# Optimization experiments

Hardware: AMD Instinct MI355X
Metric: run time of the kernel (lower is better)

The kernel has to match this reference:

```python
import jax, jax.numpy as jnp
import numpy as np

B, L, D, H, T = 1024, 50, 4, 512, 30


def _lstm_cell(x, h, c, W_ih, W_hh, b_ih, b_hh):
    # PyTorch LSTM gate order: i, f, g, o
    g = x @ W_ih.T + b_ih + h @ W_hh.T + b_hh
    i, f, gg, o = jnp.split(g, 4, axis=-1)
    c = jax.nn.sigmoid(f) * c + jax.nn.sigmoid(i) * jnp.tanh(gg)
    h = jax.nn.sigmoid(o) * jnp.tanh(c)
    return h, c


def setup_inputs() -> dict:
    key = jax.random.key(0)
    ks = jax.random.split(key, 16)
    s = 0.05
    return {
        "input_tensor": jax.random.normal(ks[0], (B, L, D), jnp.float32),
        "target_len": T,
        "enc_W_ih": jax.random.normal(ks[1], (4 * H, D), jnp.float32) * s,
        "enc_W_hh": jax.random.normal(ks[2], (4 * H, H), jnp.float32) * s,
        "enc_b_ih": jax.random.normal(ks[3], (4 * H,), jnp.float32) * s,
        "enc_b_hh": jax.random.normal(ks[4], (4 * H,), jnp.float32) * s,
        "attn_W": jax.random.normal(ks[5], (L, H + D), jnp.float32) * s,
        "attn_b": jax.random.normal(ks[6], (L,), jnp.float32) * s,
        "comb_W": jax.random.normal(ks[7], (H, H + D), jnp.float32) * s,
        "comb_b": jax.random.normal(ks[8], (H,), jnp.float32) * s,
        "dec_W_ih": jax.random.normal(ks[9], (4 * H, H), jnp.float32) * s,
        "dec_W_hh": jax.random.normal(ks[10], (4 * H, H), jnp.float32) * s,
        "dec_b_ih": jax.random.normal(ks[11], (4 * H,), jnp.float32) * s,
        "dec_b_hh": jax.random.normal(ks[12], (4 * H,), jnp.float32) * s,
        "out_W": jax.random.normal(ks[13], (D, H), jnp.float32) * s,
        "out_b": jax.random.normal(ks[14], (D,), jnp.float32) * s,
    }


def reference(input_tensor, target_len, enc_W_ih, enc_W_hh, enc_b_ih, enc_b_hh,
              attn_W, attn_b, comb_W, comb_b,
              dec_W_ih, dec_W_hh, dec_b_ih, dec_b_hh, out_W, out_b):
    b = input_tensor.shape[0]

    # ---- encoder LSTM over input_len steps ----
    def enc_step(carry, x_t):
        h, c = carry
        h, c = _lstm_cell(x_t, h, c, enc_W_ih, enc_W_hh, enc_b_ih, enc_b_hh)
        return (h, c), h

    h0 = jnp.zeros((b, H), input_tensor.dtype)
    (h_enc, c_enc), enc_hs = jax.lax.scan(enc_step, (h0, h0),
                                          jnp.swapaxes(input_tensor, 0, 1))
    encoder_outputs = jnp.swapaxes(enc_hs, 0, 1)  # [B, L, H]

    # ---- recursive attention decoder over target_len steps ----
    def dec_step(carry, _):
        h, c, x = carry
        # faithful to torch: h.reshape(h.shape[1], -1).transpose(1, 0)
        h_r = jnp.transpose(h.reshape(H, -1))  # [B, H] (memory reinterpret)
        attn_logits = jnp.concatenate([x, h_r], axis=1) @ attn_W.T + attn_b
        attn_weights = jax.nn.softmax(attn_logits, axis=1)        # [B, L]
        attn_applied = jnp.einsum('bl,blh->bh', attn_weights, encoder_outputs)
        comb = jnp.concatenate([x, attn_applied], axis=1) @ comb_W.T + comb_b
        comb = jax.nn.relu(comb)                                  # [B, H]
        h, c = _lstm_cell(comb, h, c, dec_W_ih, dec_W_hh, dec_b_ih, dec_b_hh)
        pred = h @ out_W.T + out_b                                # [B, D]
        return (h, c, pred), pred

    dec_in0 = input_tensor[:, -1, :]
    _, preds = jax.lax.scan(dec_step, (h_enc, c_enc, dec_in0), None,
                            length=target_len)
    return jnp.swapaxes(preds, 0, 1)  # [B, target_len, D]
```

## Files before the change

### kernel.cpp

```cpp
#include <hip/hip_runtime.h>
#include <hip/hip_bf16.h>

#define Bsz   1024
#define Lseq  50
#define Din   4
#define Hd    512
#define Tlen  30
#define NWG   256

typedef __hip_bfloat16 bf16;
typedef short s16x8 __attribute__((ext_vector_type(8)));
typedef short s16x4 __attribute__((ext_vector_type(4)));
typedef float f32x4 __attribute__((ext_vector_type(4)));
typedef int   i32x2 __attribute__((ext_vector_type(2)));

__device__ __forceinline__ float bf2f(bf16 x){ return __bfloat162float(x); }
__device__ __forceinline__ bf16  f2bf(float x){ return __float2bfloat16(x); }
__device__ __forceinline__ float bfbits2f(short u){
    union { unsigned int ui; float f; } v;
    v.ui = ((unsigned int)(unsigned short)u) << 16;
    return v.f;
}
__device__ __forceinline__ short f2bfbits(float x){
    bf16 h = f2bf(x); short s; __builtin_memcpy(&s, &h, 2); return s;
}
__device__ __forceinline__ float sigm(float x){ return 1.0f/(1.0f + __expf(-x)); }
__device__ __forceinline__ float ftanh(float x){
    const float e = __expf(2.0f*x);
    return 1.0f - 2.0f/(e + 1.0f);
}
__device__ __forceinline__ i32x2 pack4(float a, float b, float c, float d){
    i32x2 v;
    v[0] = (int)(unsigned short)f2bfbits(a) | ((int)(unsigned short)f2bfbits(b) << 16);
    v[1] = (int)(unsigned short)f2bfbits(c) | ((int)(unsigned short)f2bfbits(d) << 16);
    return v;
}
__device__ __forceinline__ s16x4 sc_load_b64(const void* p){
    i32x2 v;
    asm volatile("global_load_dwordx2 %0, %1, off sc0 sc1\n\ts_waitcnt vmcnt(0)"
                 : "=v"(v) : "v"(p) : "memory");
    s16x4 r; __builtin_memcpy(&r, &v, 8); return r;
}

#define OFF_ABUF0   (0u)
#define OFF_ABUF1   (2u<<20)
#define OFF_ATTNAP  (8u<<20)
#define OFF_XDEC    (9u<<20)
#define OFF_FLAG    ((9u<<20) + (16u<<10))
#define OFF_COMBWR  ((9u<<20) + (32u<<10))
#define OFF_ATTNWR  ((9u<<20) + (600u<<10))
#define OFF_FLAGS   ((9u<<20) + (704u<<10))
#define OFF_WCACHE  (10u<<20)
#define OFF_ENCOUT  (18u<<20)

#define WC_INPUT 0
#define WC_EWIH  204800
#define WC_EWHH  212992
#define WC_EBIH  1261568
#define WC_EBHH  1263616
#define WC_AW    1265664
#define WC_AB    1291464
#define WC_CW    1291520
#define WC_CB    1555712
#define WC_DWIH  1556224
#define WC_DWHH  2604800
#define WC_DBIH  3653376
#define WC_DBHH  3655424
#define WC_OW    3657472
#define WC_OB    3659520
#define WC_TOTAL 3659524

__device__ __constant__ int WOFF[15] = {
    WC_INPUT, WC_EWIH, WC_EWHH, WC_EBIH, WC_EBHH, WC_AW, WC_AB, WC_CW,
    WC_CB, WC_DWIH, WC_DWHH, WC_DBIH, WC_DBHH, WC_OW, WC_OB };
__device__ __constant__ int WNUM[15] = {
    204800, 8192, 1048576, 2048, 2048, 25800, 50, 264192,
    512, 1048576, 1048576, 2048, 2048, 2048, 4 };

struct Ptrs15 { const void* p[15]; };

__global__ void probe_kernel(const unsigned int* __restrict__ w, int* flag){
    __shared__ int cnt;
    if (threadIdx.x == 0) cnt = 0;
    __syncthreads();
    int c = 0;
    for (int i = threadIdx.x; i < 4096; i += 256){
        unsigned e = (w[i] >> 7) & 0xFFu;
        c += (e >= 0x80u) ? 1 : 0;
    }
    atomicAdd(&cnt, c);
    __syncthreads();
    if (threadIdx.x == 0) *flag = (cnt > 400) ? 1 : 0;
}

__global__ __launch_bounds__(256) void convert_kernel(
    Ptrs15 srcs, const int* __restrict__ flag, bf16* __restrict__ dst)
{
    const int f = *flag;
    for (int idx = blockIdx.x*256 + threadIdx.x; idx < WC_TOTAL;
         idx += gridDim.x*256){
        int a = 0;
#pragma unroll
        for (int j = 1; j < 15; ++j) if (idx >= WOFF[j]) a = j;
        const int local = idx - WOFF[a];
        if (local >= WNUM[a]) continue;
        bf16 v;
        if (f) v = f2bf(((const float*)srcs.p[a])[local]);
        else   v = ((const bf16*)srcs.p[a])[local];
        dst[idx] = v;
    }
}

__global__ __launch_bounds__(256) void setup_kernel(
    bf16* __restrict__ Abuf0, bf16* __restrict__ Abuf1,
    bf16* __restrict__ combWr, bf16* __restrict__ attnWr,
    const bf16* __restrict__ cWc, const bf16* __restrict__ aWc)
{
    const unsigned idx = blockIdx.x*256u + threadIdx.x;
    if (idx < (unsigned)Bsz*Hd){
        const unsigned row = idx >> 9, col = idx & (Hd-1);
        const bf16 z = f2bf(0.0f);
        Abuf0[(size_t)row*1024 + Hd + col] = z;
        Abuf1[(size_t)row*1024 + Hd + col] = z;
    }
    if (idx < (unsigned)Hd*Hd)
        combWr[idx] = cWc[(size_t)(idx >> 9)*(Hd+Din) + Din + (idx & (Hd-1))];
    if (idx < (unsigned)Lseq*Hd)
        attnWr[idx] = aWc[(size_t)(idx >> 9)*(Hd+Din) + Din + (idx & (Hd-1))];
}

struct MegaP {
    const bf16 *input, *eWih, *eWhh, *ebih, *ebhh;
    const bf16 *aW, *ab, *cW, *cb, *dWih, *dWhh, *dbih, *dbhh, *oW, *ob;
    const bf16 *combWr, *attnWr;
    bf16 *A0, *A1, *encout, *attnap, *xdec;
    int *wflag, *gflag, *xccmap;
    const int *flag;
    void *dout;
};

#define WSTRIDE 536

__global__ __launch_bounds__(512, 2) void mega_kernel(MegaP P)
{
    __shared__ short w1_lds[64*WSTRIDE];
    __shared__ short w2_lds[64*WSTRIDE];
    __shared__ short hr_s[4][Hd];
    __shared__ float ctx_s[2][4][8][64];
    __shared__ float aw_s[4][64];
    __shared__ int   xmap_s[NWG];
    __shared__ int   info_s[2];

    const int wg = blockIdx.x, tid = threadIdx.x;
    const int wave = tid >> 6, lane = tid & 63;
    const int quad = lane >> 4, l15 = lane & 15;
    const int lbase = lane & ~3;
    const int f32out = *P.flag;

    const int grp = wg & 7, rank = wg >> 3;

    int ep = 0;

    auto flag_round = [&](bool fence){
        ++ep;
        __syncthreads();
        if (tid == 0){
            if (fence) __threadfence();
            __hip_atomic_store(P.wflag + wg*16, ep, __ATOMIC_RELAXED, __HIP_MEMORY_SCOPE_SYSTEM);
        }
        if (rank == 0){
            if (tid < 32){
                int* f = P.wflag + (tid*8 + grp)*16;
                while (__hip_atomic_load(f, __ATOMIC_RELAXED, __HIP_MEMORY_SCOPE_SYSTEM) < ep)
                    __builtin_amdgcn_s_sleep(1);
            }
            __syncthreads();
            if (tid == 0)
                __hip_atomic_store(P.gflag + grp*16, ep, __ATOMIC_RELAXED, __HIP_MEMORY_SCOPE_SYSTEM);
        }
        if (tid < 8){
            int* f = P.gflag + tid*16;
            while (__hip_atomic_load(f, __ATOMIC_RELAXED, __HIP_MEMORY_SCOPE_SYSTEM) < ep)
                __builtin_amdgcn_s_sleep(1);
        }
        __syncthreads();
    };

    auto GSYNCF = [&](){
        flag_round(true);
        asm volatile("buffer_inv sc0 sc1" ::: "memory");
        __syncthreads();
    };

    if (tid == 0){
        int xcc = 0;
        asm volatile("s_getreg_b32 %0, hwreg(HW_REG_XCC_ID)" : "=s"(xcc));
        P.xccmap[wg] = xcc & 7;
    }
    GSYNCF();
    if (tid < NWG) xmap_s[tid] = P.xccmap[tid];
    __syncthreads();
    if (tid == 0){
        int ok = 1;
        for (int g = 0; g < 8; ++g){
            const int x0 = xmap_s[g];
            for (int i = 1; i < 32; ++i) ok &= (xmap_s[i*8 + g] == x0);
        }
        info_s[0] = ok;
    }
    __syncthreads();
    const int bal = info_s[0];

    auto GSYNCL = [&](){
        if (!bal){ GSYNCF(); return; }
        flag_round(true);
        asm volatile("buffer_inv" ::: "memory");
        __syncthreads();
    };
    auto XSYNC = [&](){
        if (!bal){ GSYNCF(); return; }
        ++ep;
        __syncthreads();
        if (tid == 0)
            __hip_atomic_store(P.wflag + wg*16, ep, __ATOMIC_RELAXED, __HIP_MEMORY_SCOPE_SYSTEM);
        if (tid < 32){
            int* f = P.wflag + (tid*8 + grp)*16;
            while (__hip_atomic_load(f, __ATOMIC_RELAXED, __HIP_MEMORY_SCOPE_SYSTEM) < ep)
                __builtin_amdgcn_s_sleep(1);
        }
        __syncthreads();
        asm volatile("buffer_inv" ::: "memory");
    };

    bf16* bufs[2] = { P.A0, P.A1 };

    const int bm0 = grp*128, hc0 = rank*16;
    const int wm = wave >> 1, wn = wave & 1;
    const int arow0 = bm0 + wm*32 + l15;

    int ng[2];
#pragma unroll
    for (int nf = 0; nf < 2; ++nf){
        const int n = wn*32 + nf*16 + l15;
        ng[nf] = (n & 3)*Hd + hc0 + (n >> 2);
    }

    float bias_e[2], wxv_e[2][4];
#pragma unroll
    for (int nf = 0; nf < 2; ++nf){
        bias_e[nf] = bf2f(P.ebih[ng[nf]]) + bf2f(P.ebhh[ng[nf]]);
        const s16x4 t4 = *reinterpret_cast<const s16x4*>(P.eWih + (size_t)ng[nf]*Din);
#pragma unroll
        for (int d = 0; d < 4; ++d) wxv_e[nf][d] = bfbits2f(t4[d]);
    }

    for (int i = tid; i < 64*64; i += 512){
        const int col = i >> 6, k8 = (i & 63)*8;
        const int g = (col & 3)*Hd + hc0 + (col >> 2);
        const s16x8 v = *reinterpret_cast<const s16x8*>(P.eWhh + (size_t)g*Hd + k8);
        *reinterpret_cast<s16x8*>(&w2_lds[col*WSTRIDE + k8]) = v;
    }
    __syncthreads();

    float creg[2][2][4];
#pragma unroll
    for (int a = 0; a < 2; ++a)
#pragma unroll
        for (int b = 0; b < 2; ++b)
#pragma unroll
            for (int r = 0; r < 4; ++r) creg[a][b][r] = 0.0f;

    for (int t = 0; t < Lseq; ++t){
        const bf16* Ain = bufs[t&1] + Hd;
        bf16* hout = bufs[(t+1)&1] + Hd;

        f32x4 acc[2][2];
#pragma unroll
        for (int mf=0; mf<2; ++mf)
#pragma unroll
            for (int nf=0; nf<2; ++nf) acc[mf][nf] = (f32x4)0.0f;

        s16x8 afr[2], bfr[2];
#pragma unroll
        for (int sl = 0; sl < 16; ++sl){
#pragma unroll
            for (int mf = 0; mf < 2; ++mf)
                afr[mf] = *reinterpret_cast<const s16x8*>(
                    Ain + (size_t)(arow0 + mf*16)*1024 + sl*32 + quad*8);
#pragma unroll
            for (int nf = 0; nf < 2; ++nf){
                const int nl = wn*32 + nf*16 + l15;
                bfr[nf] = *reinterpret_cast<const s16x8*>(
                    &w2_lds[nl*WSTRIDE + sl*32 + quad*8]);
            }
#pragma unroll
            for (int mf = 0; mf < 2; ++mf)
#pragma unroll
                for (int nf = 0; nf < 2; ++nf)
                    acc[mf][nf] = __builtin_amdgcn_mfma_f32_16x16x32_bf16(
                        afr[mf], bfr[nf], acc[mf][nf], 0, 0, 0);
        }

#pragma unroll
        for (int mf = 0; mf < 2; ++mf){
#pragma unroll
            for (int r = 0; r < 4; ++r){
                const int m = bm0 + wm*32 + mf*16 + quad*4 + r;
                const s16x4 xt = *reinterpret_cast<const s16x4*>(
                    P.input + ((size_t)m*Lseq + t)*Din);
                float xv[4];
#pragma unroll
                for (int d = 0; d < 4; ++d) xv[d] = bfbits2f(xt[d]);
#pragma unroll
                for (int nf = 0; nf < 2; ++nf){
                    const int n_loc = wn*32 + nf*16 + l15;
                    float gv = acc[mf][nf][r] + bias_e[nf]
                             + xv[0]*wxv_e[nf][0] + xv[1]*wxv_e[nf][1]
                             + xv[2]*wxv_e[nf][2] + xv[3]*wxv_e[nf][3];
                    const float gi = __shfl(gv, lbase+0);
                    const float gf = __shfl(gv, lbase+1);
                    const float gg = __shfl(gv, lbase+2);
                    const float go = __shfl(gv, lbase+3);
                    if ((lane & 3) == 0){
                        const int hcol = hc0 + (n_loc >> 2);
                        const float cn = sigm(gf)*creg[mf][nf][r] + sigm(gi)*ftanh(gg);
                        creg[mf][nf][r] = cn;
                        const float hv = sigm(go)*ftanh(cn);
                        const bf16 hb = f2bf(hv);
                        hout[(size_t)m*1024 + hcol] = hb;
                        P.encout[((size_t)m*Lseq + t)*Hd + hcol] = hb;
                    }
                }
            }
        }
        if (t == Lseq-1) GSYNCL(); else XSYNC();
    }

    for (int i = tid; i < 64*64; i += 512){
        const int col = i >> 6, k8 = (i & 63)*8;
        const int g = (col & 3)*Hd + hc0 + (col >> 2);
        *reinterpret_cast<s16x8*>(&w1_lds[col*WSTRIDE + k8]) =
            *reinterpret_cast<const s16x8*>(P.dWih + (size_t)g*Hd + k8);
        *reinterpret_cast<s16x8*>(&w2_lds[col*WSTRIDE + k8]) =
            *reinterpret_cast<const s16x8*>(P.dWhh + (size_t)g*Hd + k8);
    }

    float bias_d[2];
#pragma unroll
    for (int nf = 0; nf < 2; ++nf)
        bias_d[nf] = bf2f(P.dbih[ng[nf]]) + bf2f(P.dbhh[ng[nf]]);

    const int b0 = grp*128 + rank*4;
    const int s_uni = b0 >> 9;
    const int p0 = b0 & (Hd-1);

    const int rr = wave & 3, half = wave >> 2;
    s16x8 ereg[25];
    {
        const bf16* eb = P.encout + (size_t)(b0 + rr)*Lseq*Hd + lane*8;
#pragma unroll
        for (int i = 0; i < 25; ++i)
            ereg[i] = *reinterpret_cast<const s16x8*>(eb + (size_t)(half*25 + i)*Hd);
    }

    const int ccol = hc0 + l15;
    float bias_c, wxv_c[4];
    {
        bias_c = bf2f(P.cb[ccol]);
        const s16x4 t4 = *reinterpret_cast<const s16x4*>(P.cW + (size_t)ccol*(Hd+Din));
#pragma unroll
        for (int d = 0; d < 4; ++d) wxv_c[d] = bfbits2f(t4[d]);
    }
    __syncthreads();

    for (int t = 0; t < Tlen; ++t){
        const int p = t & 1;
        const bf16* hprev = bufs[p] + Hd;

        {
            const s16x4 hv = sc_load_b64(hprev + (size_t)(2*tid + s_uni)*1024 + p0);
            hr_s[0][tid] = hv[0]; hr_s[1][tid] = hv[1];
            hr_s[2][tid] = hv[2]; hr_s[3][tid] = hv[3];
        }
        __syncthreads();

        if (wave < 4){
            const int b = b0 + wave;
            float x0, x1, x2, x3;
            if (t == 0){
                const bf16* xp = P.input + ((size_t)b*Lseq + (Lseq-1))*Din;
                x0 = bf2f(xp[0]); x1 = bf2f(xp[1]); x2 = bf2f(xp[2]); x3 = bf2f(xp[3]);
            } else {
                float q0=0.f, q1=0.f, q2=0.f, q3=0.f;
                const bf16* hb = hprev + (size_t)b*1024;
                for (int k = lane; k < Hd; k += 64){
                    const float hv = bf2f(hb[k]);
                    q0 += hv*bf2f(P.oW[k]);
                    q1 += hv*bf2f(P.oW[Hd+k]);
                    q2 += hv*bf2f(P.oW[2*Hd+k]);
                    q3 += hv*bf2f(P.oW[3*Hd+k]);
                }
#pragma unroll
                for (int off = 32; off; off >>= 1){
                    q0 += __shfl_down(q0, off); q1 += __shfl_down(q1, off);
                    q2 += __shfl_down(q2, off); q3 += __shfl_down(q3, off);
                }
                x0 = __shfl(q0,0) + bf2f(P.ob[0]);
                x1 = __shfl(q1,0) + bf2f(P.ob[1]);
                x2 = __shfl(q2,0) + bf2f(P.ob[2]);
                x3 = __shfl(q3,0) + bf2f(P.ob[3]);
                if (lane == 0){
                    const size_t o = ((size_t)b*Tlen + (t-1))*Din;
                    if (f32out){
                        float* dp = (float*)P.dout + o;
                        dp[0]=x0; dp[1]=x1; dp[2]=x2; dp[3]=x3;
                    } else {
                        *reinterpret_cast<i32x2*>((bf16*)P.dout + o) = pack4(x0,x1,x2,x3);
                    }
                }
            }
            if (lane == 0)
                *reinterpret_cast<i32x2*>(P.xdec + (size_t)b*Din) = pack4(x0,x1,x2,x3);

            float logit = -3.0e38f;
            if (lane < Lseq){
                float a0 = bf2f(P.ab[lane]);
                {
                    const bf16* wx = P.aW + (size_t)lane*(Hd+Din);
                    a0 += x0*bf2f(wx[0]) + x1*bf2f(wx[1]) + x2*bf2f(wx[2]) + x3*bf2f(wx[3]);
                }
                float a1 = 0.f, a2 = 0.f, a3 = 0.f;
                const bf16* wr = P.attnWr + (size_t)lane*Hd;
                for (int j = 0; j < Hd; j += 16){
                    float t4[4] = {0.f,0.f,0.f,0.f};
#pragma unroll
                    for (int q = 0; q < 4; ++q){
                        const s16x4 hw = *reinterpret_cast<const s16x4*>(&hr_s[wave][j + q*4]);
                        const s16x4 wv = *reinterpret_cast<const s16x4*>(wr + j + q*4);
                        t4[q] = bfbits2f(hw[0])*bfbits2f(wv[0]) + bfbits2f(hw[1])*bfbits2f(wv[1])
                              + bfbits2f(hw[2])*bfbits2f(wv[2]) + bfbits2f(hw[3])*bfbits2f(wv[3]);
                    }
                    a0 += t4[0]; a1 += t4[1]; a2 += t4[2]; a3 += t4[3];
                }
                logit = (a0 + a1) + (a2 + a3);
            }
            float mx = logit;
#pragma unroll
            for (int off = 32; off; off >>= 1) mx = fmaxf(mx, __shfl_xor(mx, off));
            const float e = (lane < Lseq) ? __expf(logit - mx) : 0.0f;
            float se = e;
#pragma unroll
            for (int off = 32; off; off >>= 1) se += __shfl_xor(se, off);
            aw_s[wave][lane] = e / se;
        }
        __syncthreads();

        {
            float acc8[8] = {0.f,0.f,0.f,0.f,0.f,0.f,0.f,0.f};
#pragma unroll
            for (int i = 0; i < 25; ++i){
                const float w = aw_s[rr][half*25 + i];
#pragma unroll
                for (int q = 0; q < 8; ++q) acc8[q] += w * bfbits2f(ereg[i][q]);
            }
#pragma unroll
            for (int q = 0; q < 8; ++q) ctx_s[half][rr][q][lane] = acc8[q];
        }
        __syncthreads();

        if (wave < 4){
            const int b = b0 + wave;
            s16x8 ov;
#pragma unroll
            for (int q = 0; q < 8; ++q)
                ov[q] = f2bfbits(ctx_s[0][wave][q][lane] + ctx_s[1][wave][q][lane]);
            *reinterpret_cast<s16x8*>(P.attnap + (size_t)b*Hd + lane*8) = ov;
        }
        XSYNC();

        {
            f32x4 cacc = (f32x4)0.0f;
            const bf16* Ab = P.attnap + (size_t)(bm0 + wave*16 + l15)*Hd + quad*8;
#pragma unroll
            for (int kk = 0; kk < 16; ++kk){
                const s16x8 bfr = *reinterpret_cast<const s16x8*>(
                    P.combWr + (size_t)ccol*Hd + kk*32 + quad*8);
                const s16x8 afr2 = *reinterpret_cast<const s16x8*>(Ab + kk*32);
                cacc = __builtin_amdgcn_mfma_f32_16x16x32_bf16(afr2, bfr, cacc, 0, 0, 0);
            }
            bf16* outp = bufs[p];
#pragma unroll
            for (int r = 0; r < 4; ++r){
                const int m = bm0 + wave*16 + quad*4 + r;
                const s16x4 xt = *reinterpret_cast<const s16x4*>(P.xdec + (size_t)m*Din);
                float v = cacc[r] + bias_c
                        + bfbits2f(xt[0])*wxv_c[0] + bfbits2f(xt[1])*wxv_c[1]
                        + bfbits2f(xt[2])*wxv_c[2] + bfbits2f(xt[3])*wxv_c[3];
                v = fmaxf(v, 0.0f);
                outp[(size_t)m*1024 + ccol] = f2bf(v);
            }
        }
        XSYNC();

        {
            const bf16* Ain = bufs[p];
            bf16* hout = bufs[p^1] + Hd;
            f32x4 acc[2][2];
#pragma unroll
            for (int mf=0; mf<2; ++mf)
#pragma unroll
                for (int nf=0; nf<2; ++nf) acc[mf][nf] = (f32x4)0.0f;

            s16x8 afr[2], bfr[2];
#pragma unroll
            for (int sl = 0; sl < 16; ++sl){
#pragma unroll
                for (int mf = 0; mf < 2; ++mf)
                    afr[mf] = *reinterpret_cast<const s16x8*>(
                        Ain + (size_t)(arow0 + mf*16)*1024 + sl*32 + quad*8);
#pragma unroll
                for (int nf = 0; nf < 2; ++nf){
                    const int nl = wn*32 + nf*16 + l15;
                    bfr[nf] = *reinterpret_cast<const s16x8*>(
                        &w1_lds[nl*WSTRIDE + sl*32 + quad*8]);
                }
#pragma unroll
                for (int mf = 0; mf < 2; ++mf)
#pragma unroll
                    for (int nf = 0; nf < 2; ++nf)
                        acc[mf][nf] = __builtin_amdgcn_mfma_f32_16x16x32_bf16(
                            afr[mf], bfr[nf], acc[mf][nf], 0, 0, 0);
            }
#pragma unroll
            for (int sl = 0; sl < 16; ++sl){
#pragma unroll
                for (int mf = 0; mf < 2; ++mf)
                    afr[mf] = *reinterpret_cast<const s16x8*>(
                        Ain + (size_t)(arow0 + mf*16)*1024 + Hd + sl*32 + quad*8);
#pragma unroll
                for (int nf = 0; nf < 2; ++nf){
                    const int nl = wn*32 + nf*16 + l15;
                    bfr[nf] = *reinterpret_cast<const s16x8*>(
                        &w2_lds[nl*WSTRIDE + sl*32 + quad*8]);
                }
#pragma unroll
                for (int mf = 0; mf < 2; ++mf)
#pragma unroll
                    for (int nf = 0; nf < 2; ++nf)
                        acc[mf][nf] = __builtin_amdgcn_mfma_f32_16x16x32_bf16(
                            afr[mf], bfr[nf], acc[mf][nf], 0, 0, 0);
            }

#pragma unroll
            for (int mf = 0; mf < 2; ++mf){
#pragma unroll
                for (int r = 0; r < 4; ++r){
                    const int m = bm0 + wm*32 + mf*16 + quad*4 + r;
#pragma unroll
                    for (int nf = 0; nf < 2; ++nf){
                        const int n_loc = wn*32 + nf*16 + l15;
                        float gv = acc[mf][nf][r] + bias_d[nf];
                        const float gi = __shfl(gv, lbase+0);
                        const float gf = __shfl(gv, lbase+1);
                        const float gg = __shfl(gv, lbase+2);
                        const float go = __shfl(gv, lbase+3);
                        if ((lane & 3) == 0){
                            const int hcol = hc0 + (n_loc >> 2);
                            const float cn = sigm(gf)*creg[mf][nf][r] + sigm(gi)*ftanh(gg);
                            creg[mf][nf][r] = cn;
                            const float hv = sigm(go)*ftanh(cn);
                            hout[(size_t)m*1024 + hcol] = f2bf(hv);
                        }
                    }
                }
            }
        }
        GSYNCL();
    }

    if (wave < 4){
        const int b = b0 + wave;
        const bf16* hb = bufs[Tlen & 1] + Hd + (size_t)b*1024;
        float q0=0.f, q1=0.f, q2=0.f, q3=0.f;
        for (int k = lane; k < Hd; k += 64){
            const float hv = bf2f(hb[k]);
            q0 += hv*bf2f(P.oW[k]);
            q1 += hv*bf2f(P.oW[Hd+k]);
            q2 += hv*bf2f(P.oW[2*Hd+k]);
            q3 += hv*bf2f(P.oW[3*Hd+k]);
        }
#pragma unroll
        for (int off = 32; off; off >>= 1){
            q0 += __shfl_down(q0, off); q1 += __shfl_down(q1, off);
            q2 += __shfl_down(q2, off); q3 += __shfl_down(q3, off);
        }
        if (lane == 0){
            const size_t o = ((size_t)b*Tlen + (Tlen-1))*Din;
            const float r0 = q0 + bf2f(P.ob[0]), r1 = q1 + bf2f(P.ob[1]);
            const float r2 = q2 + bf2f(P.ob[2]), r3 = q3 + bf2f(P.ob[3]);
            if (f32out){
                float* dp = (float*)P.dout + o;
                dp[0]=r0; dp[1]=r1; dp[2]=r2; dp[3]=r3;
            } else {
                *reinterpret_cast<i32x2*>((bf16*)P.dout + o) = pack4(r0,r1,r2,r3);
            }
        }
    }
}

extern "C" void kernel_launch(void* const* d_in, const int* in_sizes, int n_in,
                              void* d_out, int out_size, void* d_ws, size_t ws_size,
                              hipStream_t stream)
{
    char* ws = (char*)d_ws;
    bf16*  Abuf0   = (bf16*)(ws + OFF_ABUF0);
    bf16*  Abuf1   = (bf16*)(ws + OFF_ABUF1);
    bf16*  attnap  = (bf16*)(ws + OFF_ATTNAP);
    bf16*  xdec    = (bf16*)(ws + OFF_XDEC);
    int*   flag    = (int*)(ws + OFF_FLAG);
    bf16*  combWr  = (bf16*)(ws + OFF_COMBWR);
    bf16*  attnWr  = (bf16*)(ws + OFF_ATTNWR);
    int*   flags   = (int*)(ws + OFF_FLAGS);
    bf16*  wc      = (bf16*)(ws + OFF_WCACHE);
    bf16*  enc_out = (bf16*)(ws + OFF_ENCOUT);

    hipMemsetAsync(flags, 0, 20480, stream);

    probe_kernel<<<1, 256, 0, stream>>>((const unsigned int*)d_in[3], flag);

    Ptrs15 srcs;
    srcs.p[0]=d_in[0];  srcs.p[1]=d_in[2];  srcs.p[2]=d_in[3];  srcs.p[3]=d_in[4];
    srcs.p[4]=d_in[5];  srcs.p[5]=d_in[6];  srcs.p[6]=d_in[7];  srcs.p[7]=d_in[8];
    srcs.p[8]=d_in[9];  srcs.p[9]=d_in[10]; srcs.p[10]=d_in[11];srcs.p[11]=d_in[12];
    srcs.p[12]=d_in[13];srcs.p[13]=d_in[14];srcs.p[14]=d_in[15];
    convert_kernel<<<1024, 256, 0, stream>>>(srcs, flag, wc);

    setup_kernel<<<2048, 256, 0, stream>>>(Abuf0, Abuf1, combWr, attnWr,
                                           wc+WC_CW, wc+WC_AW);

    MegaP P;
    P.input = wc+WC_INPUT; P.eWih = wc+WC_EWIH; P.eWhh = wc+WC_EWHH;
    P.ebih = wc+WC_EBIH;   P.ebhh = wc+WC_EBHH;
    P.aW = wc+WC_AW;  P.ab = wc+WC_AB;  P.cW = wc+WC_CW;  P.cb = wc+WC_CB;
    P.dWih = wc+WC_DWIH; P.dWhh = wc+WC_DWHH; P.dbih = wc+WC_DBIH; P.dbhh = wc+WC_DBHH;
    P.oW = wc+WC_OW;  P.ob = wc+WC_OB;
    P.combWr = combWr; P.attnWr = attnWr;
    P.A0 = Abuf0; P.A1 = Abuf1; P.encout = enc_out; P.attnap = attnap; P.xdec = xdec;
    P.wflag = flags; P.gflag = flags + 256*16; P.xccmap = flags + 256*16 + 8*16;
    P.flag = flag; P.dout = d_out;

    mega_kernel<<<NWG, 512, 0, stream>>>(P);
}
```

Baseline: 3.524 ms.

## Write transposed hidden-state copy so decoder h reshape reads are coalesced

The LSTM epilogues now write an extra transposed, bf16-pair-packed copy of the hidden state (hT0/hT1) using cache-bypassing stores. This lets the decoder's reshape/transpose reads of h for attention be done with contiguous 8-byte loads instead of strided gathers across 1024-element rows. The epilogue is also restructured so each lane computes the cell math for four rows before the lane-masked stores, which removes divergence around the transcendental math. In exchange there are extra global stores every decoder step, and correctness depends on the transposed index mapping matching the original strided reshape.

```diff
diff --git a/kernel.cpp b/kernel.cpp
--- a/kernel.cpp
+++ b/kernel.cpp
@@ -35,15 +35,23 @@
     v[1] = (int)(unsigned short)f2bfbits(c) | ((int)(unsigned short)f2bfbits(d) << 16);
     return v;
 }
+__device__ __forceinline__ int pack2(float a, float b){
+    return (int)(unsigned short)f2bfbits(a) | ((int)(unsigned short)f2bfbits(b) << 16);
+}
 __device__ __forceinline__ s16x4 sc_load_b64(const void* p){
     i32x2 v;
     asm volatile("global_load_dwordx2 %0, %1, off sc0 sc1\n\ts_waitcnt vmcnt(0)"
                  : "=v"(v) : "v"(p) : "memory");
     s16x4 r; __builtin_memcpy(&r, &v, 8); return r;
 }
+__device__ __forceinline__ void sc_store_b32(void* p, int v){
+    asm volatile("global_store_dword %0, %1, off sc0 sc1" :: "v"(p), "v"(v) : "memory");
+}
 
 #define OFF_ABUF0   (0u)
 #define OFF_ABUF1   (2u<<20)
+#define OFF_HT0     (4u<<20)
+#define OFF_HT1     (5u<<20)
 #define OFF_ATTNAP  (8u<<20)
 #define OFF_XDEC    (9u<<20)
 #define OFF_FLAG    ((9u<<20) + (16u<<10))
@@ -134,6 +142,7 @@
     const bf16 *aW, *ab, *cW, *cb, *dWih, *dWhh, *dbih, *dbhh, *oW, *ob;
     const bf16 *combWr, *attnWr;
     bf16 *A0, *A1, *encout, *attnap, *xdec;
+    bf16 *hT0, *hT1;
     int *wflag, *gflag, *xccmap;
     const int *flag;
     void *dout;
@@ -303,32 +312,42 @@
 
 #pragma unroll
         for (int mf = 0; mf < 2; ++mf){
-#pragma unroll
-            for (int r = 0; r < 4; ++r){
-                const int m = bm0 + wm*32 + mf*16 + quad*4 + r;
-                const s16x4 xt = *reinterpret_cast<const s16x4*>(
-                    P.input + ((size_t)m*Lseq + t)*Din);
-                float xv[4];
-#pragma unroll
-                for (int d = 0; d < 4; ++d) xv[d] = bfbits2f(xt[d]);
-#pragma unroll
-                for (int nf = 0; nf < 2; ++nf){
-                    const int n_loc = wn*32 + nf*16 + l15;
+            const int mb = bm0 + wm*32 + mf*16 + quad*4;
+            s16x4 xts[4];
+#pragma unroll
+            for (int r = 0; r < 4; ++r)
+                xts[r] = *reinterpret_cast<const s16x4*>(
+                    P.input + ((size_t)(mb+r)*Lseq + t)*Din);
+#pragma unroll
+            for (int nf = 0; nf < 2; ++nf){
+                const int n_loc = wn*32 + nf*16 + l15;
+                float hvv[4];
+#pragma unroll
+                for (int r = 0; r < 4; ++r){
                     float gv = acc[mf][nf][r] + bias_e[nf]
-                             + xv[0]*wxv_e[nf][0] + xv[1]*wxv_e[nf][1]
-                             + xv[2]*wxv_e[nf][2] + xv[3]*wxv_e[nf][3];
+                             + bfbits2f(xts[r][0])*wxv_e[nf][0]
+                             + bfbits2f(xts[r][1])*wxv_e[nf][1]
+                             + bfbits2f(xts[r][2])*wxv_e[nf][2]
+                             + bfbits2f(xts[r][3])*wxv_e[nf][3];
                     const float gi = __shfl(gv, lbase+0);
                     const float gf = __shfl(gv, lbase+1);
                     const float gg = __shfl(gv, lbase+2);
                     const float go = __shfl(gv, lbase+3);
-                    if ((lane & 3) == 0){
-                        const int hcol = hc0 + (n_loc >> 2);
-                        const float cn = sigm(gf)*creg[mf][nf][r] + sigm(gi)*ftanh(gg);
-                        creg[mf][nf][r] = cn;
-                        const float hv = sigm(go)*ftanh(cn);
-                        const bf16 hb = f2bf(hv);
-                        hout[(size_t)m*1024 + hcol] = hb;
-                        P.encout[((size_t)m*Lseq + t)*Hd + hcol] = hb;
+                    const float cn = sigm(gf)*creg[mf][nf][r] + sigm(gi)*ftanh(gg);
+                    creg[mf][nf][r] = cn;
+                    hvv[r] = sigm(go)*ftanh(cn);
+                }
+                if ((lane & 3) == 0){
+                    const int hcol = hc0 + (n_loc >> 2);
+#pragma unroll
+                    for (int r = 0; r < 4; ++r){
+                        const bf16 hb = f2bf(hvv[r]);
+                        hout[(size_t)(mb+r)*1024 + hcol] = hb;
+                        P.encout[((size_t)(mb+r)*Lseq + t)*Hd + hcol] = hb;
+                    }
+                    if (t == Lseq-1){
+                        sc_store_b32(P.hT1 + ((hcol*2+0)<<9) + (mb>>1), pack2(hvv[0], hvv[2]));
+                        sc_store_b32(P.hT1 + ((hcol*2+1)<<9) + (mb>>1), pack2(hvv[1], hvv[3]));
                     }
                 }
             }
@@ -378,9 +397,11 @@
         const bf16* hprev = bufs[p] + Hd;
 
         {
-            const s16x4 hv = sc_load_b64(hprev + (size_t)(2*tid + s_uni)*1024 + p0);
-            hr_s[0][tid] = hv[0]; hr_s[1][tid] = hv[1];
-            hr_s[2][tid] = hv[2]; hr_s[3][tid] = hv[3];
+            const bf16* hTr = (t & 1) ? P.hT0 : P.hT1;
+            const int q = tid >> 7;
+            const int i0 = (tid & 127) << 2;
+            const s16x4 hv = sc_load_b64(hTr + (size_t)(((p0 + q)*2 + s_uni)<<9) + i0);
+            *reinterpret_cast<s16x4*>(&hr_s[q][i0]) = hv;
         }
         __syncthreads();
 
@@ -505,6 +526,7 @@
         {
             const bf16* Ain = bufs[p];
             bf16* hout = bufs[p^1] + Hd;
+            bf16* hTw = (t & 1) ? P.hT1 : P.hT0;
             f32x4 acc[2][2];
 #pragma unroll
             for (int mf=0; mf<2; ++mf)
@@ -553,24 +575,29 @@
 
 #pragma unroll
             for (int mf = 0; mf < 2; ++mf){
-#pragma unroll
-                for (int r = 0; r < 4; ++r){
-                    const int m = bm0 + wm*32 + mf*16 + quad*4 + r;
-#pragma unroll
-                    for (int nf = 0; nf < 2; ++nf){
-                        const int n_loc = wn*32 + nf*16 + l15;
+                const int mb = bm0 + wm*32 + mf*16 + quad*4;
+#pragma unroll
+                for (int nf = 0; nf < 2; ++nf){
+                    const int n_loc = wn*32 + nf*16 + l15;
+                    float hvv[4];
+#pragma unroll
+                    for (int r = 0; r < 4; ++r){
                         float gv = acc[mf][nf][r] + bias_d[nf];
                         const float gi = __shfl(gv, lbase+0);
                         const float gf = __shfl(gv, lbase+1);
                         const float gg = __shfl(gv, lbase+2);
                         const float go = __shfl(gv, lbase+3);
-                        if ((lane & 3) == 0){
-                            const int hcol = hc0 + (n_loc >> 2);
-                            const float cn = sigm(gf)*creg[mf][nf][r] + sigm(gi)*ftanh(gg);
-                            creg[mf][nf][r] = cn;
-                            const float hv = sigm(go)*ftanh(cn);
-                            hout[(size_t)m*1024 + hcol] = f2bf(hv);
-                        }
+                        const float cn = sigm(gf)*creg[mf][nf][r] + sigm(gi)*ftanh(gg);
+                        creg[mf][nf][r] = cn;
+                        hvv[r] = sigm(go)*ftanh(cn);
+                    }
+                    if ((lane & 3) == 0){
+                        const int hcol = hc0 + (n_loc >> 2);
+#pragma unroll
+                        for (int r = 0; r < 4; ++r)
+                            hout[(size_t)(mb+r)*1024 + hcol] = f2bf(hvv[r]);
+                        sc_store_b32(hTw + ((hcol*2+0)<<9) + (mb>>1), pack2(hvv[0], hvv[2]));
+                        sc_store_b32(hTw + ((hcol*2+1)<<9) + (mb>>1), pack2(hvv[1], hvv[3]));
                     }
                 }
             }
@@ -615,6 +642,8 @@
     char* ws = (char*)d_ws;
     bf16*  Abuf0   = (bf16*)(ws + OFF_ABUF0);
     bf16*  Abuf1   = (bf16*)(ws + OFF_ABUF1);
+    bf16*  hT0     = (bf16*)(ws + OFF_HT0);
+    bf16*  hT1     = (bf16*)(ws + OFF_HT1);
     bf16*  attnap  = (bf16*)(ws + OFF_ATTNAP);
     bf16*  xdec    = (bf16*)(ws + OFF_XDEC);
     int*   flag    = (int*)(ws + OFF_FLAG);
@@ -646,7 +675,9 @@
     P.oW = wc+WC_OW;  P.ob = wc+WC_OB;
     P.combWr = combWr; P.attnWr = attnWr;
     P.A0 = Abuf0; P.A1 = Abuf1; P.encout = enc_out; P.attnap = attnap; P.xdec = xdec;
-    P.wflag = flags; P.gflag = flags + 256*16; P.xccmap = flags + 256*16 + 8*16;
+    P.hT0 = hT0; P.hT1 = hT1;
+    P.wflag = flags; P.gflag = flags + 256*16;
+    P.xccmap = flags + 256*16 + 8*16;
     P.flag = flag; P.dout = d_out;
 
     mega_kernel<<<NWG, 512, 0, stream>>>(P);
```

Result: faster. 3.435 ms (-2.5%).
